# Optimization experiments

Measured on AMD Instinct MI355X. Metric: run time of the kernel, lower is better.

The kernel has to match this reference:

```python
import jax, jax.numpy as jnp
import numpy as np

B, C, H, W = 16, 512, 64, 64


def setup_inputs() -> dict:
    key = jax.random.key(0)
    ks = jax.random.split(key, 8)
    s = 1.0 / np.sqrt(C)  # fan-in scale like torch conv default
    return {
        "x": jax.random.normal(ks[0], (B, C, H, W), dtype=jnp.float32),
        "y": jax.random.normal(ks[1], (B, C), dtype=jnp.float32),
        "wq": jax.random.normal(ks[2], (C, C), dtype=jnp.float32) * s,
        "bq": jax.random.normal(ks[3], (C,), dtype=jnp.float32) * s,
        "wk": jax.random.normal(ks[4], (C, C), dtype=jnp.float32) * s,
        "bk": jax.random.normal(ks[5], (C,), dtype=jnp.float32) * s,
        "wv": jax.random.normal(ks[6], (C, C), dtype=jnp.float32) * s,
        "bv": jax.random.normal(ks[7], (C,), dtype=jnp.float32) * s,
        "gamma": jnp.ones((1,), dtype=jnp.float32),
    }


def _conv1x1_flat(inp_flat, w, b):
    # inp_flat: (B, C, N); 1x1 conv == per-pixel channel GEMM
    return jnp.einsum("oc,bcn->bon", w, inp_flat) + b[None, :, None]


def reference(x, y, wq, bq, wk, bk, wv, bv, gamma):
    b, c, h, w = x.shape
    n = h * w
    # align=True: y (B, C) broadcast to (B, C, H, W); flatten spatial dims
    y_flat = jnp.broadcast_to(y[:, :, None], (b, c, n))
    x_flat = x.reshape(b, c, n)
    # exchange=False: q = y, k = v = x
    pq = _conv1x1_flat(y_flat, wq, bq)          # (B, C, N)
    pk = _conv1x1_flat(x_flat, wk, bk)          # (B, C, N)
    pv = _conv1x1_flat(x_flat, wv, bv)          # (B, C, N)
    energy = jnp.einsum("bcn,bdn->bcd", pq, pk)  # (B, C, C) channel attention
    attn = jax.nn.softmax(energy, axis=-1)
    out = jnp.einsum("bcd,bdn->bcn", attn, pv)   # (B, C, N)
    out = out.reshape(b, c, h, w)
    return gamma * out + x
```

## Files before the change

### kernel.cpp

```cpp
#include <hip/hip_runtime.h>
#include <hip/hip_bf16.h>

#define Bn 16
#define Cn 512
#define Nn 4096

typedef unsigned short u16;
typedef __bf16 bf16x8 __attribute__((ext_vector_type(8)));
typedef float f32x4 __attribute__((ext_vector_type(4)));
typedef unsigned short u16x8 __attribute__((ext_vector_type(8)));

__device__ __forceinline__ u16 f2bf(float f) {
    __hip_bfloat16 h = __float2bfloat16(f);
    return *reinterpret_cast<u16*>(&h);
}

__device__ __forceinline__ void glds16(const u16* g, u16* l) {
    __builtin_amdgcn_global_load_lds(
        (const __attribute__((address_space(1))) void*)g,
        (__attribute__((address_space(3))) void*)l, 16, 0, 0);
}

__global__ __launch_bounds__(256) void k_transpose(
    const float* __restrict__ x, u16* __restrict__ xt, float* __restrict__ sxp)
{
    __shared__ float tile[128 * 65];
    const int b = blockIdx.z, c0 = blockIdx.y * 128, n0 = blockIdx.x * 64;
    const int t = threadIdx.x;
    const float* xb = x + ((size_t)(b * Cn + c0)) * Nn + n0;

    float part[8];
#pragma unroll
    for (int r = 0; r < 8; ++r) {
        int cl = (t >> 4) + r * 16;
        int nl = (t & 15) * 4;
        float4 v = *(const float4*)(xb + (size_t)cl * Nn + nl);
        float* tp = &tile[cl * 65 + nl];
        tp[0] = v.x; tp[1] = v.y; tp[2] = v.z; tp[3] = v.w;
        part[r] = (v.x + v.y) + (v.z + v.w);
    }
#pragma unroll
    for (int m = 1; m < 16; m <<= 1) {
#pragma unroll
        for (int r = 0; r < 8; ++r) part[r] += __shfl_xor(part[r], m);
    }
    if ((t & 15) == 0) {
#pragma unroll
        for (int r = 0; r < 8; ++r) {
            int cl = (t >> 4) + r * 16;
            sxp[(size_t)(b * Cn + c0 + cl) * 64 + blockIdx.x] = part[r];
        }
    }
    __syncthreads();
    u16* xtb = xt + ((size_t)(b * Nn + n0)) * Cn + c0;
#pragma unroll
    for (int r = 0; r < 4; ++r) {
        int nl = (t >> 4) + r * 16;
        int c8 = (t & 15) * 8;
        u16x8 hv;
#pragma unroll
        for (int i = 0; i < 8; ++i) hv[i] = f2bf(tile[(c8 + i) * 65 + nl]);
        *(u16x8*)(xtb + (size_t)nl * Cn + c8) = hv;
    }
}

__global__ __launch_bounds__(256) void k_sxred(
    const float* __restrict__ sxp, float* __restrict__ sx)
{
    int i = blockIdx.x * 256 + threadIdx.x;
    const float4* p = (const float4*)(sxp + (size_t)i * 64);
    float s = 0.f;
#pragma unroll
    for (int j = 0; j < 16; ++j) {
        float4 v = p[j];
        s += (v.x + v.y) + (v.z + v.w);
    }
    sx[i] = s;
}

__global__ __launch_bounds__(256) void k_qk(
    const float* __restrict__ wq, const float* __restrict__ bq,
    const float* __restrict__ wk, const float* __restrict__ bk,
    const float* __restrict__ y, const float* __restrict__ sx,
    float* __restrict__ qy, float* __restrict__ sk)
{
    const int w = threadIdx.x >> 6, lane = threadIdx.x & 63;
    const int o = blockIdx.x * 4 + w;
    const int b = blockIdx.y;
    const int mode = blockIdx.z;
    const float* W = mode ? wk : wq;
    const float* vec = mode ? (sx + b * Cn) : (y + b * Cn);
    float sum = 0.f;
#pragma unroll
    for (int i = 0; i < 8; ++i) {
        int k2 = lane + i * 64;
        sum += W[(size_t)o * Cn + k2] * vec[k2];
    }
#pragma unroll
    for (int m = 1; m < 64; m <<= 1) sum += __shfl_xor(sum, m);
    if (lane == 0) {
        if (mode) sk[b * Cn + o] = sum + 4096.0f * bk[o];
        else      qy[b * Cn + o] = sum + bq[o];
    }
}

__global__ __launch_bounds__(256) void k_wvt(
    const float* __restrict__ wv, u16* __restrict__ wvt)
{
    __shared__ float tl[64 * 65];
    const int d0 = blockIdx.x * 64, e0 = blockIdx.y * 64;
    const int t = threadIdx.x;
#pragma unroll
    for (int r = 0; r < 4; ++r) {
        int d = (t >> 4) + r * 16, e4 = (t & 15) * 4;
        float4 v = *(const float4*)(wv + (size_t)(d0 + d) * Cn + e0 + e4);
        float* p = &tl[d * 65 + e4];
        p[0] = v.x; p[1] = v.y; p[2] = v.z; p[3] = v.w;
    }
    __syncthreads();
#pragma unroll
    for (int r = 0; r < 4; ++r) {
        int e = (t >> 4) + r * 16, d4 = (t & 15) * 4;
        ushort4 h;
        h.x = f2bf(tl[(d4 + 0) * 65 + e]);
        h.y = f2bf(tl[(d4 + 1) * 65 + e]);
        h.z = f2bf(tl[(d4 + 2) * 65 + e]);
        h.w = f2bf(tl[(d4 + 3) * 65 + e]);
        *(ushort4*)(wvt + (size_t)(e0 + e) * Cn + d0 + d4) = h;
    }
}

__global__ __launch_bounds__(256) void k_softmax(
    const float* __restrict__ qy, const float* __restrict__ sk,
    const float* __restrict__ bv, u16* __restrict__ attn,
    float* __restrict__ beff, const float* __restrict__ gamma)
{
    __shared__ float red[4], red2[4], red3[4];
    const int b = blockIdx.x >> 9, c = blockIdx.x & 511;
    const int t = threadIdx.x;
    const float q = qy[b * Cn + c];
    const float l0 = q * sk[b * Cn + t];
    const float l1 = q * sk[b * Cn + t + 256];
    float mx = fmaxf(l0, l1);
#pragma unroll
    for (int m = 1; m < 64; m <<= 1) mx = fmaxf(mx, __shfl_xor(mx, m));
    if ((t & 63) == 0) red[t >> 6] = mx;
    __syncthreads();
    mx = fmaxf(fmaxf(red[0], red[1]), fmaxf(red[2], red[3]));
    const float e0 = __expf(l0 - mx), e1 = __expf(l1 - mx);
    float s = e0 + e1;
#pragma unroll
    for (int m = 1; m < 64; m <<= 1) s += __shfl_xor(s, m);
    if ((t & 63) == 0) red2[t >> 6] = s;
    __syncthreads();
    s = red2[0] + red2[1] + red2[2] + red2[3];
    const float inv = 1.0f / s;
    const float a0 = e0 * inv, a1 = e1 * inv;
    u16* arow = attn + ((size_t)(b * Cn + c)) * Cn;
    arow[t] = f2bf(a0);
    arow[t + 256] = f2bf(a1);
    float pb = a0 * bv[t] + a1 * bv[t + 256];
#pragma unroll
    for (int m = 1; m < 64; m <<= 1) pb += __shfl_xor(pb, m);
    if ((t & 63) == 0) red3[t >> 6] = pb;
    __syncthreads();
    if (t == 0)
        beff[b * Cn + c] = gamma[0] * (red3[0] + red3[1] + red3[2] + red3[3]);
}

template <int FINAL>
__global__ __launch_bounds__(256) void k_gemm(
    const u16* __restrict__ A, size_t strideA,
    const u16* __restrict__ Bt, size_t strideB,
    int N,
    u16* __restrict__ outBf, size_t strideOb,
    float* __restrict__ outF,
    const float* __restrict__ xres,
    const float* __restrict__ beff,
    const float* __restrict__ gamma)
{
    constexpr int K = 512;
    __shared__ float smem_f[8448];
    u16* la = (u16*)smem_f;
    u16* lb = la + 128 * 64;
    const int b = blockIdx.z;
    const int m0 = blockIdx.y * 128;
    const int n0 = blockIdx.x * 128;
    A  += (size_t)b * strideA;
    Bt += (size_t)b * strideB;
    const int t = threadIdx.x;
    const int lane = t & 63;
    const int w = t >> 6;
    const int wm = (w >> 1) * 64, wn = (w & 1) * 64;
    const int l15 = lane & 15, quad = lane >> 4;

    f32x4 acc[4][4];
#pragma unroll
    for (int i = 0; i < 4; ++i)
#pragma unroll
        for (int j = 0; j < 4; ++j)
            acc[i][j] = (f32x4){0.f, 0.f, 0.f, 0.f};

    const int srow8 = lane >> 3;
    const int lgcol = ((lane & 7) ^ srow8) * 8;

    for (int k0 = 0; k0 < K; k0 += 64) {
        __syncthreads();
#pragma unroll
        for (int j = 0; j < 4; ++j) {
            const int row = w * 32 + j * 8 + srow8;
            const int sb = (w * 256 + j * 64) * 8;
            glds16(A  + (size_t)(m0 + row) * K + k0 + lgcol, la + sb);
            glds16(Bt + (size_t)(n0 + row) * K + k0 + lgcol, lb + sb);
        }
        __syncthreads();

#pragma unroll
        for (int kk2 = 0; kk2 < 2; ++kk2) {
            bf16x8 af[4], bfr[4];
#pragma unroll
            for (int mi = 0; mi < 4; ++mi) {
                const int r = wm + mi * 16 + l15;
                const int pg = ((kk2 << 2) + quad) ^ (l15 & 7);
                af[mi] = *(const bf16x8*)&la[r * 64 + pg * 8];
            }
#pragma unroll
            for (int ni = 0; ni < 4; ++ni) {
                const int r = wn + ni * 16 + l15;
                const int pg = ((kk2 << 2) + quad) ^ (l15 & 7);
                bfr[ni] = *(const bf16x8*)&lb[r * 64 + pg * 8];
            }
#pragma unroll
            for (int mi = 0; mi < 4; ++mi)
#pragma unroll
                for (int ni = 0; ni < 4; ++ni)
                    acc[mi][ni] = __builtin_amdgcn_mfma_f32_16x16x32_bf16(
                        af[mi], bfr[ni], acc[mi][ni], 0, 0, 0);
        }
    }

    if (FINAL) {
        float* lc = smem_f;
#pragma unroll
        for (int h = 0; h < 2; ++h) {
            __syncthreads();
            if ((w >> 1) == h) {
#pragma unroll
                for (int mi = 0; mi < 4; ++mi)
#pragma unroll
                    for (int reg = 0; reg < 4; ++reg) {
                        const int rl = mi * 16 + quad * 4 + reg;
#pragma unroll
                        for (int ni = 0; ni < 4; ++ni)
                            lc[rl * 132 + wn + ni * 16 + l15] = acc[mi][ni][reg];
                    }
            }
            __syncthreads();
            const int rb = h * 64;
#pragma unroll
            for (int rr = 0; rr < 8; ++rr) {
                const int rl = rr * 8 + (t >> 5);
                const int c4 = (t & 31) * 4;
                float4 v = *(float4*)&lc[rl * 132 + c4];
                const int r = m0 + rb + rl;
                const float be = beff[b * Cn + r];
                const size_t base = ((size_t)(b * Cn + r)) * N + n0 + c4;
                float4 xr = *(const float4*)(xres + base);
                float4 o;
                o.x = (v.x + be) + xr.x;
                o.y = (v.y + be) + xr.y;
                o.z = (v.z + be) + xr.z;
                o.w = (v.w + be) + xr.w;
                *(float4*)(outF + base) = o;
            }
        }
    } else {
        const float gs = gamma[0];
#pragma unroll
        for (int mi = 0; mi < 4; ++mi) {
#pragma unroll
            for (int reg = 0; reg < 4; ++reg) {
                const int r = m0 + wm + mi * 16 + quad * 4 + reg;
                const size_t base = (size_t)b * strideOb + (size_t)r * N;
#pragma unroll
                for (int ni = 0; ni < 4; ++ni) {
                    const int cidx = n0 + wn + ni * 16 + l15;
                    outBf[base + cidx] = f2bf(gs * acc[mi][ni][reg]);
                }
            }
        }
    }
}

__global__ __launch_bounds__(512, 4) void k_gemm2(
    const u16* __restrict__ A,
    const u16* __restrict__ Bt,
    float* __restrict__ outF,
    const float* __restrict__ xres,
    const float* __restrict__ beff)
{
    extern __shared__ u16 sm[];
    const int b = blockIdx.z;
    const int m0 = blockIdx.y << 8;
    const int n0 = blockIdx.x << 7;
    const int t = threadIdx.x;
    const int lane = t & 63, w = t >> 6;
    const int wm = (w >> 1) << 6, wn = (w & 1) << 6;
    const int l15 = lane & 15, quad = lane >> 4;

    const u16* Ag = A + (size_t)b * Cn * Cn;
    const u16* Bg = Bt + (size_t)b * ((size_t)Nn * Cn);
    const int srow = t >> 2;
    const int scol = (((t & 3) ^ ((srow >> 1) & 3))) << 3;
    const u16* pa = Ag + (size_t)(m0 + srow) * Cn + scol;
    const u16* pb = Bg + (size_t)(n0 + srow) * Cn + scol;
    u16* dw = sm + w * 512;

#define SLOTO(s) ((s) * 12288)
#define STGA(s, c, k0) \
    glds16(pa + (size_t)(c) * (128 * Cn) + (k0), dw + SLOTO(s) + (c) * 4096)
#define STGB(s, k0) glds16(pb + (k0), dw + SLOTO(s) + 8192)
#define FRG(base, row, qd) \
    (*(const bf16x8*)&sm[(base) + (row) * 32 + \
                         (((qd) ^ (((row) >> 1) & 3)) << 3)])

    f32x4 acc[4][4];
#pragma unroll
    for (int mi = 0; mi < 4; ++mi)
#pragma unroll
        for (int reg = 0; reg < 4; ++reg) {
            const int row = m0 + wm + mi * 16 + quad * 4 + reg;
            const float* xr =
                xres + ((size_t)(b * Cn + row)) * Nn + n0 + wn + l15;
#pragma unroll
            for (int ni = 0; ni < 4; ++ni)
                acc[mi][ni][reg] = xr[ni * 16];
        }
    asm volatile("" ::: "memory");
    __builtin_amdgcn_sched_barrier(0);

    STGA(0, 0, 0); STGA(0, 1, 0); STGB(0, 0);
    STGA(1, 0, 32); STGA(1, 1, 32); STGB(1, 32);

#pragma unroll
    for (int tI = 0; tI < 16; ++tI) {
        if (tI < 15) { asm volatile("s_waitcnt vmcnt(3)" ::: "memory"); }
        else         { asm volatile("s_waitcnt vmcnt(0)" ::: "memory"); }
        __builtin_amdgcn_s_barrier();
        if (tI <= 13) {
            const int s2 = (tI + 2) % 3;
            const int k2 = (tI + 2) << 5;
            STGA(s2, 0, k2); STGA(s2, 1, k2); STGB(s2, k2);
        }
        const int sb = SLOTO(tI % 3);
        bf16x8 af[4], bf[4];
#pragma unroll
        for (int mi = 0; mi < 4; ++mi)
            af[mi] = FRG(sb, wm + mi * 16 + l15, quad);
#pragma unroll
        for (int ni = 0; ni < 4; ++ni)
            bf[ni] = FRG(sb + 8192, wn + ni * 16 + l15, quad);
        __builtin_amdgcn_s_setprio(1);
#pragma unroll
        for (int mi = 0; mi < 4; ++mi)
#pragma unroll
            for (int ni = 0; ni < 4; ++ni)
                acc[mi][ni] = __builtin_amdgcn_mfma_f32_16x16x32_bf16(
                    af[mi], bf[ni], acc[mi][ni], 0, 0, 0);
        __builtin_amdgcn_s_setprio(0);
    }
#undef STGA
#undef STGB
#undef FRG
#undef SLOTO

    __syncthreads();
    float* lc = (float*)sm;
#pragma unroll
    for (int h = 0; h < 4; ++h) {
        if (h) __syncthreads();
        if ((w >> 1) == h) {
#pragma unroll
            for (int mi = 0; mi < 4; ++mi)
#pragma unroll
                for (int reg = 0; reg < 4; ++reg) {
                    const int rl = mi * 16 + quad * 4 + reg;
#pragma unroll
                    for (int ni = 0; ni < 4; ++ni)
                        lc[rl * 132 + wn + ni * 16 + l15] = acc[mi][ni][reg];
                }
        }
        __syncthreads();
#pragma unroll
        for (int k = 0; k < 4; ++k) {
            const int r = (t >> 5) + k * 16;
            const int c4 = (t & 31) * 4;
            float4 v = *(float4*)&lc[r * 132 + c4];
            const int row = m0 + h * 64 + r;
            const float be = beff[b * Cn + row];
            const size_t base = ((size_t)(b * Cn + row)) * Nn + n0 + c4;
            float4 o;
            o.x = v.x + be;
            o.y = v.y + be;
            o.z = v.z + be;
            o.w = v.w + be;
            *(float4*)(outF + base) = o;
        }
    }
}

extern "C" void kernel_launch(void* const* d_in, const int* in_sizes, int n_in,
                              void* d_out, int out_size, void* d_ws, size_t ws_size,
                              hipStream_t stream)
{
    const float* x     = (const float*)d_in[0];
    const float* y     = (const float*)d_in[1];
    const float* wq    = (const float*)d_in[2];
    const float* bq    = (const float*)d_in[3];
    const float* wk    = (const float*)d_in[4];
    const float* bk    = (const float*)d_in[5];
    const float* wv    = (const float*)d_in[6];
    const float* bv    = (const float*)d_in[7];
    const float* gamma = (const float*)d_in[8];
    float* out = (float*)d_out;

    char* ws = (char*)d_ws;
    u16*   xt   = (u16*)  (ws + 0);
    float* sxp  = (float*)(ws + 67108864);
    float* sx   = (float*)(ws + 69206016);
    float* qy   = (float*)(ws + 69238784);
    float* sk   = (float*)(ws + 69271552);
    float* beff = (float*)(ws + 69304320);
    u16*   attn = (u16*)  (ws + 69337088);
    u16*   wvt  = (u16*)  (ws + 77725696);
    u16*   weff = (u16*)  (ws + 78249984);

    k_transpose<<<dim3(64, 4, Bn), dim3(256), 0, stream>>>(x, xt, sxp);
    k_sxred<<<dim3(32), dim3(256), 0, stream>>>(sxp, sx);
    k_wvt<<<dim3(8, 8), dim3(256), 0, stream>>>(wv, wvt);
    k_qk<<<dim3(128, Bn, 2), dim3(256), 0, stream>>>(wq, bq, wk, bk, y, sx, qy, sk);
    k_softmax<<<dim3(Bn * Cn), dim3(256), 0, stream>>>(qy, sk, bv, attn, beff, gamma);
    k_gemm<0><<<dim3(4, 4, Bn), dim3(256), 0, stream>>>(
        attn, (size_t)Cn * Cn, wvt, (size_t)0, Cn,
        weff, (size_t)Cn * Cn, nullptr, nullptr, nullptr, gamma);
    if (hipFuncSetAttribute((const void*)k_gemm2,
                            hipFuncAttributeMaxDynamicSharedMemorySize,
                            73728) == hipSuccess) {
        k_gemm2<<<dim3(32, 2, Bn), dim3(512), 73728, stream>>>(
            weff, xt, out, x, beff);
    } else {
        k_gemm<1><<<dim3(32, 4, Bn), dim3(256), 0, stream>>>(
            weff, (size_t)Cn * Cn, xt, (size_t)Nn * Cn, Nn,
            nullptr, (size_t)0, out, x, beff, gamma);
    }
}
```

Baseline: 353.4 us.

## Deepen B-operand prefetch to four stages and use nontemporal output stores

Splits the shared-memory ring in the main GEMM so the A tiles keep a 3-slot ring while the B (xt) tiles get a 4-slot ring, prefetched three iterations ahead instead of two. The vmcnt waits are adjusted to match. The goal is to hide more global-load latency for the streamed operand. It also switches the output write to nontemporal stores to avoid polluting cache, at the cost of raising dynamic LDS from 72 KB to 80 KB per block, which may reduce occupancy.

```diff
diff --git a/kernel.cpp b/kernel.cpp
--- a/kernel.cpp
+++ b/kernel.cpp
@@ -314,14 +314,17 @@
     const int scol = (((t & 3) ^ ((srow >> 1) & 3))) << 3;
     const u16* pa = Ag + (size_t)(m0 + srow) * Cn + scol;
     const u16* pb = Bg + (size_t)(n0 + srow) * Cn + scol;
-    u16* dw = sm + w * 512;
-
-#define SLOTO(s) ((s) * 12288)
+    const int dwo = w * 512;
+
 #define STGA(s, c, k0) \
-    glds16(pa + (size_t)(c) * (128 * Cn) + (k0), dw + SLOTO(s) + (c) * 4096)
-#define STGB(s, k0) glds16(pb + (k0), dw + SLOTO(s) + 8192)
-#define FRG(base, row, qd) \
-    (*(const bf16x8*)&sm[(base) + (row) * 32 + \
+    glds16(pa + (size_t)(c) * (128 * Cn) + (k0), \
+           sm + (s) * 8192 + (c) * 4096 + dwo)
+#define STGB(s, k0) glds16(pb + (k0), sm + 24576 + (s) * 4096 + dwo)
+#define FRGA(s, row, qd) \
+    (*(const bf16x8*)&sm[(s) * 8192 + (row) * 32 + \
+                         (((qd) ^ (((row) >> 1) & 3)) << 3)])
+#define FRGB(s, row, qd) \
+    (*(const bf16x8*)&sm[24576 + (s) * 4096 + (row) * 32 + \
                          (((qd) ^ (((row) >> 1) & 3)) << 3)])
 
     f32x4 acc[4][4];
@@ -339,27 +342,33 @@
     asm volatile("" ::: "memory");
     __builtin_amdgcn_sched_barrier(0);
 
-    STGA(0, 0, 0); STGA(0, 1, 0); STGB(0, 0);
-    STGA(1, 0, 32); STGA(1, 1, 32); STGB(1, 32);
+    STGB(0, 0);
+    STGA(0, 0, 0); STGA(0, 1, 0);
+    STGB(1, 32);
+    STGA(1, 0, 32); STGA(1, 1, 32);
+    STGB(2, 64);
 
 #pragma unroll
     for (int tI = 0; tI < 16; ++tI) {
-        if (tI < 15) { asm volatile("s_waitcnt vmcnt(3)" ::: "memory"); }
-        else         { asm volatile("s_waitcnt vmcnt(0)" ::: "memory"); }
+        if (tI <= 13)      { asm volatile("s_waitcnt vmcnt(4)" ::: "memory"); }
+        else if (tI == 14) { asm volatile("s_waitcnt vmcnt(3)" ::: "memory"); }
+        else               { asm volatile("s_waitcnt vmcnt(0)" ::: "memory"); }
         __builtin_amdgcn_s_barrier();
-        if (tI <= 13) {
-            const int s2 = (tI + 2) % 3;
-            const int k2 = (tI + 2) << 5;
-            STGA(s2, 0, k2); STGA(s2, 1, k2); STGB(s2, k2);
-        }
-        const int sb = SLOTO(tI % 3);
+        if (tI + 2 <= 15) {
+            STGA((tI + 2) % 3, 0, (tI + 2) << 5);
+            STGA((tI + 2) % 3, 1, (tI + 2) << 5);
+        }
+        if (tI + 3 <= 15) {
+            STGB((tI + 3) & 3, (tI + 3) << 5);
+        }
+        const int sa = tI % 3, sb4 = tI & 3;
         bf16x8 af[4], bf[4];
 #pragma unroll
         for (int mi = 0; mi < 4; ++mi)
-            af[mi] = FRG(sb, wm + mi * 16 + l15, quad);
+            af[mi] = FRGA(sa, wm + mi * 16 + l15, quad);
 #pragma unroll
         for (int ni = 0; ni < 4; ++ni)
-            bf[ni] = FRG(sb + 8192, wn + ni * 16 + l15, quad);
+            bf[ni] = FRGB(sb4, wn + ni * 16 + l15, quad);
         __builtin_amdgcn_s_setprio(1);
 #pragma unroll
         for (int mi = 0; mi < 4; ++mi)
@@ -371,8 +380,8 @@
     }
 #undef STGA
 #undef STGB
-#undef FRG
-#undef SLOTO
+#undef FRGA
+#undef FRGB
 
     __syncthreads();
     float* lc = (float*)sm;
@@ -395,16 +404,16 @@
         for (int k = 0; k < 4; ++k) {
             const int r = (t >> 5) + k * 16;
             const int c4 = (t & 31) * 4;
-            float4 v = *(float4*)&lc[r * 132 + c4];
+            f32x4 v = *(f32x4*)&lc[r * 132 + c4];
             const int row = m0 + h * 64 + r;
             const float be = beff[b * Cn + row];
             const size_t base = ((size_t)(b * Cn + row)) * Nn + n0 + c4;
-            float4 o;
-            o.x = v.x + be;
-            o.y = v.y + be;
-            o.z = v.z + be;
-            o.w = v.w + be;
-            *(float4*)(outF + base) = o;
+            f32x4 o;
+            o[0] = v[0] + be;
+            o[1] = v[1] + be;
+            o[2] = v[2] + be;
+            o[3] = v[3] + be;
+            __builtin_nontemporal_store(o, (f32x4*)(outF + base));
         }
     }
 }
@@ -445,8 +454,8 @@
         weff, (size_t)Cn * Cn, nullptr, nullptr, nullptr, gamma);
     if (hipFuncSetAttribute((const void*)k_gemm2,
                             hipFuncAttributeMaxDynamicSharedMemorySize,
-                            73728) == hipSuccess) {
-        k_gemm2<<<dim3(32, 2, Bn), dim3(512), 73728, stream>>>(
+                            81920) == hipSuccess) {
+        k_gemm2<<<dim3(32, 2, Bn), dim3(512), 81920, stream>>>(
             weff, xt, out, x, beff);
     } else {
         k_gemm<1><<<dim3(32, 4, Bn), dim3(256), 0, stream>>>(
```

Measured after the change: 331.6 us. 6.2% less time.
